# Optimization experiments

Hardware: AMD Instinct MI355X
Metric: run time of the kernel (lower is better)

## Reference

```python
import jax, jax.numpy as jnp
import numpy as np

B, T, I, H = 4096, 512, 3, 64


def setup_inputs() -> dict:
    key = jax.random.key(0)
    ks = jax.random.split(key, 8)
    s = 1.0 / np.sqrt(H)  # PyTorch LSTM init scale
    x = jax.random.normal(ks[0], (B, T, I), dtype=jnp.float32)
    W_ih = jax.random.uniform(ks[1], (4 * H, I), minval=-s, maxval=s, dtype=jnp.float32)
    W_hh = jax.random.uniform(ks[2], (4 * H, H), minval=-s, maxval=s, dtype=jnp.float32)
    b_ih = jax.random.uniform(ks[3], (4 * H,), minval=-s, maxval=s, dtype=jnp.float32)
    b_hh = jax.random.uniform(ks[4], (4 * H,), minval=-s, maxval=s, dtype=jnp.float32)
    W_dec = jax.random.uniform(ks[5], (I, H), minval=-s, maxval=s, dtype=jnp.float32)
    b_dec = jax.random.uniform(ks[6], (I,), minval=-s, maxval=s, dtype=jnp.float32)
    return {"x": x, "W_ih": W_ih, "W_hh": W_hh, "b_ih": b_ih, "b_hh": b_hh,
            "W_dec": W_dec, "b_dec": b_dec}


def _lstm(x, W_ih, W_hh, b_ih, b_hh):
    # Precompute input contribution for all timesteps: [B, T, 4H]
    x_gates = jnp.einsum('bti,gi->btg', x, W_ih) + b_ih + b_hh
    h0 = jnp.zeros((x.shape[0], H), dtype=x.dtype)
    c0 = jnp.zeros((x.shape[0], H), dtype=x.dtype)

    def step(carry, xg_t):
        h, c = carry
        gates = xg_t + h @ W_hh.T  # [B, 4H]
        i_g, f_g, g_g, o_g = jnp.split(gates, 4, axis=-1)  # PyTorch order i,f,g,o
        i_g = jax.nn.sigmoid(i_g)
        f_g = jax.nn.sigmoid(f_g)
        g_g = jnp.tanh(g_g)
        o_g = jax.nn.sigmoid(o_g)
        c_new = f_g * c + i_g * g_g
        h_new = o_g * jnp.tanh(c_new)
        return (h_new, c_new), h_new

    _, hs = jax.lax.scan(step, (h0, c0), jnp.swapaxes(x_gates, 0, 1))  # [T, B, H]
    return jnp.swapaxes(hs, 0, 1)  # [B, T, H]


def reference(x, W_ih, W_hh, b_ih, b_hh, W_dec, b_dec):
    lstm_out = _lstm(x, W_ih, W_hh, b_ih, b_hh)
    return jnp.einsum('bth,oh->bto', lstm_out, W_dec) + b_dec  # [B, T, I]
```

## Files before the change

kernel.cpp:

```cpp
#include <hip/hip_runtime.h>


#define TLEN 512
#define TCHUNK 64
#define ROWS 16

typedef float    float4_t __attribute__((ext_vector_type(4)));
typedef _Float16 halfx8   __attribute__((ext_vector_type(8)));

#define INV2048 4.8828125e-4f

__device__ __forceinline__ float fexp2(float x){ return __builtin_amdgcn_exp2f(x); }
__device__ __forceinline__ float frcp (float x){ return __builtin_amdgcn_rcpf(x); }
__device__ __forceinline__ float sigm (float x){ return frcp(1.f + fexp2(-1.44269504f*x)); }
__device__ __forceinline__ float tanh_(float x){ return 1.f - 2.f*frcp(1.f + fexp2(2.88539008f*x)); }

__device__ __forceinline__ unsigned short hbits(_Float16 h){
  union { _Float16 h; unsigned short u; } x; x.h = h; return x.u;
}

__device__ __forceinline__ void split8h(const float* v, halfx8& hi, halfx8& lo){
  #pragma unroll
  for (int j = 0; j < 8; j++){
    _Float16 h = (_Float16)v[j];
    hi[j] = h;
    lo[j] = (_Float16)((v[j] - (float)h) * 2048.0f);
  }
}

#define MFMA(a,b,c) __builtin_amdgcn_mfma_f32_16x16x32_f16((a),(b),(c),0,0,0)

#define HHI 0
#define HS_SZ 2304
#define XOF 0
#define XPK 3136
#define OOF 7232
#define LF_SZ 10368

__global__ __launch_bounds__(256, 1)
void LSTMAnomalyDetector_kernel(
    const float* __restrict__ x,     const float* __restrict__ W_ih,
    const float* __restrict__ W_hh,  const float* __restrict__ b_ih,
    const float* __restrict__ b_hh,  const float* __restrict__ W_dec,
    const float* __restrict__ b_dec, float* __restrict__ out)
{
  __shared__ __align__(16) unsigned short HS[HS_SZ];
  __shared__ __align__(16) float          LF[LF_SZ];

  const int tid  = threadIdx.x;
  const int w    = tid >> 6;
  const int lane = tid & 63;
  const int q    = lane >> 4;
  const int lid  = lane & 15;
  const int b0   = blockIdx.x * ROWS;
  const int cw   = w*16 + lid;

  halfx8 Bh[4][2], Bl[4][2];
  halfx8 Dh[2];
  float  wi[4][3], bsum[4];

  #pragma unroll
  for (int tl = 0; tl < 4; tl++){
    const int g = tl*64 + cw;
    #pragma unroll
    for (int kt = 0; kt < 2; kt++){
      const float* p = W_hh + g*64 + kt*32 + q*8;
      float v[8];
      #pragma unroll
      for (int j = 0; j < 8; j++) v[j] = p[j];
      split8h(v, Bh[tl][kt], Bl[tl][kt]);
    }
    wi[tl][0] = W_ih[g*3+0];
    wi[tl][1] = W_ih[g*3+1];
    wi[tl][2] = W_ih[g*3+2];
    bsum[tl]  = b_ih[g] + b_hh[g];
  }
  #pragma unroll
  for (int kt = 0; kt < 2; kt++){
    #pragma unroll
    for (int j = 0; j < 8; j++) Dh[kt][j] = (_Float16)0.f;
    if (lid < 3){
      const float* p = W_dec + lid*64 + kt*32 + q*8;
      #pragma unroll
      for (int j = 0; j < 8; j++) Dh[kt][j] = (_Float16)p[j];
    }
  }
  const float bdec = (lid < 3) ? b_dec[lid] : 0.f;

  halfx8 ah0 = {}, ah1 = {};
  float creg[4] = {0.f, 0.f, 0.f, 0.f};
  float4_t xp4[4];

  auto loadx = [&](int d){
    #pragma unroll
    for (int r = 0; r < 4; r++){
      float4_t xv = *(const float4_t*)&LF[XPK + d*64 + (q*4+r)*4];
      #pragma unroll
      for (int tl = 0; tl < 4; tl++)
        xp4[tl][r] = fmaf(wi[tl][2], xv[2],
                      fmaf(wi[tl][1], xv[1],
                        fmaf(wi[tl][0], xv[0], bsum[tl])));
    }
  };

  auto step = [&](int t, int dt, bool last){
    const int hb = (t & 1) * 1152;

    float4_t c1 = xp4[3];
    c1 = MFMA(ah0, Bh[3][0], c1);
    c1 = MFMA(ah1, Bh[3][1], c1);
    float4_t c2 = {0.f,0.f,0.f,0.f};
    c2 = MFMA(ah0, Bl[3][0], c2);
    c2 = MFMA(ah1, Bl[3][1], c2);
    float4_t og;
    #pragma unroll
    for (int r = 0; r < 4; r++) og[r] = sigm(fmaf(c2[r], INV2048, c1[r]));

    c1 = xp4[1];
    c1 = MFMA(ah0, Bh[1][0], c1);
    c1 = MFMA(ah1, Bh[1][1], c1);
    c2 = (float4_t){0.f,0.f,0.f,0.f};
    c2 = MFMA(ah0, Bl[1][0], c2);
    c2 = MFMA(ah1, Bl[1][1], c2);
    float4_t cp;
    #pragma unroll
    for (int r = 0; r < 4; r++){
      const float fg = sigm(fmaf(c2[r], INV2048, c1[r]));
      cp[r] = fg * creg[r];
    }

    c1 = xp4[0];
    c1 = MFMA(ah0, Bh[0][0], c1);
    c1 = MFMA(ah1, Bh[0][1], c1);
    c2 = (float4_t){0.f,0.f,0.f,0.f};
    c2 = MFMA(ah0, Bl[0][0], c2);
    c2 = MFMA(ah1, Bl[0][1], c2);
    float4_t ig;
    #pragma unroll
    for (int r = 0; r < 4; r++) ig[r] = sigm(fmaf(c2[r], INV2048, c1[r]));

    c1 = xp4[2];
    c1 = MFMA(ah0, Bh[2][0], c1);
    c1 = MFMA(ah1, Bh[2][1], c1);
    c2 = (float4_t){0.f,0.f,0.f,0.f};
    c2 = MFMA(ah0, Bl[2][0], c2);
    c2 = MFMA(ah1, Bl[2][1], c2);
    #pragma unroll
    for (int r = 0; r < 4; r++){
      const float gg = tanh_(fmaf(c2[r], INV2048, c1[r]));
      creg[r] = fmaf(ig[r], gg, cp[r]);
      const float h = og[r] * tanh_(creg[r]);
      const _Float16 h16 = (_Float16)h;
      HS[HHI + hb + (q*4+r)*72 + cw] = hbits(h16);
    }

    if (!last) loadx(dt+1);

    __syncthreads();

    {
      const unsigned short* ph = &HS[HHI + hb + lid*72 + q*8];
      ah0 = *(const halfx8*)&ph[0];
      ah1 = *(const halfx8*)&ph[32];
    }

    if (w == 0){
      float4_t d1 = {0.f,0.f,0.f,0.f};
      d1 = MFMA(ah0, Dh[0], d1);
      d1 = MFMA(ah1, Dh[1], d1);
      if (lid < 3){
        #pragma unroll
        for (int r = 0; r < 4; r++)
          LF[OOF + (q*4+r)*196 + dt*3 + lid] = d1[r] + bdec;
      }
    }
  };

  #pragma unroll
  for (int s = 0; s < 3; s++){
    const int f = tid + 256*s;
    const int row = f/48; const int off = (f%48)*4;
    float4_t v = *(const float4_t*)(x + (size_t)(b0+row)*1536 + off);
    *(float4_t*)&LF[XOF + row*196 + off] = v;
  }
  __syncthreads();
  #pragma unroll
  for (int s = 0; s < 4; s++){
    const int p = tid + 256*s;
    const float* xr = &LF[XOF + (p & 15)*196 + (p >> 4)*3];
    float4_t v = {xr[0], xr[1], xr[2], 0.f};
    *(float4_t*)&LF[XPK + p*4] = v;
  }
  __syncthreads();
  loadx(0);

  for (int ck = 0; ck < TLEN/TCHUNK; ++ck){
    const int tb = ck * TCHUNK;

    for (int dt = 0; dt < TCHUNK-1; ++dt)
      step(tb + dt, dt, false);

    step(tb + TCHUNK-1, TCHUNK-1, true);

    __syncthreads();
    #pragma unroll
    for (int s = 0; s < 3; s++){
      const int f = tid + 256*s;
      const int row = f/48; const int off = (f%48)*4;
      float4_t v = *(const float4_t*)&LF[OOF + row*196 + off];
      *(float4_t*)(out + (size_t)(b0+row)*1536 + tb*3 + off) = v;
    }
    if (ck + 1 < TLEN/TCHUNK){
      const int tn = tb + TCHUNK;
      #pragma unroll
      for (int s = 0; s < 3; s++){
        const int f = tid + 256*s;
        const int row = f/48; const int off = (f%48)*4;
        float4_t v = *(const float4_t*)(x + (size_t)(b0+row)*1536 + tn*3 + off);
        *(float4_t*)&LF[XOF + row*196 + off] = v;
      }
      __syncthreads();
      #pragma unroll
      for (int s = 0; s < 4; s++){
        const int p = tid + 256*s;
        const float* xr = &LF[XOF + (p & 15)*196 + (p >> 4)*3];
        float4_t v = {xr[0], xr[1], xr[2], 0.f};
        *(float4_t*)&LF[XPK + p*4] = v;
      }
    }
    __syncthreads();
    if (ck + 1 < TLEN/TCHUNK) loadx(0);
  }
}

extern "C" void kernel_launch(void* const* d_in, const int* in_sizes, int n_in,
                              void* d_out, int out_size, void* d_ws, size_t ws_size,
                              hipStream_t stream)
{
  const float* x     = (const float*)d_in[0];
  const float* W_ih  = (const float*)d_in[1];
  const float* W_hh  = (const float*)d_in[2];
  const float* b_ih  = (const float*)d_in[3];
  const float* b_hh  = (const float*)d_in[4];
  const float* W_dec = (const float*)d_in[5];
  const float* b_dec = (const float*)d_in[6];
  float* out = (float*)d_out;

  const int B = in_sizes[0] / (TLEN * 3);
  const int blocks = B / ROWS;
  hipLaunchKernelGGL(LSTMAnomalyDetector_kernel, dim3(blocks), dim3(256), 0, stream,
                     x, W_ih, W_hh, b_ih, b_hh, W_dec, b_dec, out);
}
```

Measured before the change: 448.0 us.

## Add dedicated decoder warp and double-buffer output to overlap with recurrence

Adds a fifth wavefront that computes the decoder projection for the previous timestep from the shared h buffer, taking that MFMA and store off wave 0's critical path. The output staging area is double-buffered, so a finished chunk is written to global memory lazily at the start of the next chunk instead of at a barrier. In exchange, block size grows to 320 threads and LDS use increases. The extra wave also joins every per-step barrier.

Result: faster. 426.0 us (-4.9%).

```diff
diff --git a/kernel.cpp b/kernel.cpp
--- a/kernel.cpp
+++ b/kernel.cpp
@@ -34,10 +34,11 @@
 #define HS_SZ 2304
 #define XOF 0
 #define XPK 3136
-#define OOF 7232
-#define LF_SZ 10368
-
-__global__ __launch_bounds__(256, 1)
+#define OOF0 7232
+#define OOF1 10368
+#define LF_SZ 13504
+
+__global__ __launch_bounds__(320, 1)
 void LSTMAnomalyDetector_kernel(
     const float* __restrict__ x,     const float* __restrict__ W_ih,
     const float* __restrict__ W_hh,  const float* __restrict__ b_ih,
@@ -53,36 +54,39 @@
   const int q    = lane >> 4;
   const int lid  = lane & 15;
   const int b0   = blockIdx.x * ROWS;
-  const int cw   = w*16 + lid;
+  const int cw   = (w & 3)*16 + lid;
 
   halfx8 Bh[4][2], Bl[4][2];
   halfx8 Dh[2];
   float  wi[4][3], bsum[4];
 
-  #pragma unroll
-  for (int tl = 0; tl < 4; tl++){
-    const int g = tl*64 + cw;
+  if (w < 4){
+    #pragma unroll
+    for (int tl = 0; tl < 4; tl++){
+      const int g = tl*64 + cw;
+      #pragma unroll
+      for (int kt = 0; kt < 2; kt++){
+        const float* p = W_hh + g*64 + kt*32 + q*8;
+        float v[8];
+        #pragma unroll
+        for (int j = 0; j < 8; j++) v[j] = p[j];
+        split8h(v, Bh[tl][kt], Bl[tl][kt]);
+      }
+      wi[tl][0] = W_ih[g*3+0];
+      wi[tl][1] = W_ih[g*3+1];
+      wi[tl][2] = W_ih[g*3+2];
+      bsum[tl]  = b_ih[g] + b_hh[g];
+    }
+  } else {
     #pragma unroll
     for (int kt = 0; kt < 2; kt++){
-      const float* p = W_hh + g*64 + kt*32 + q*8;
-      float v[8];
-      #pragma unroll
-      for (int j = 0; j < 8; j++) v[j] = p[j];
-      split8h(v, Bh[tl][kt], Bl[tl][kt]);
-    }
-    wi[tl][0] = W_ih[g*3+0];
-    wi[tl][1] = W_ih[g*3+1];
-    wi[tl][2] = W_ih[g*3+2];
-    bsum[tl]  = b_ih[g] + b_hh[g];
-  }
-  #pragma unroll
-  for (int kt = 0; kt < 2; kt++){
-    #pragma unroll
-    for (int j = 0; j < 8; j++) Dh[kt][j] = (_Float16)0.f;
-    if (lid < 3){
-      const float* p = W_dec + lid*64 + kt*32 + q*8;
-      #pragma unroll
-      for (int j = 0; j < 8; j++) Dh[kt][j] = (_Float16)p[j];
+      #pragma unroll
+      for (int j = 0; j < 8; j++) Dh[kt][j] = (_Float16)0.f;
+      if (lid < 3){
+        const float* p = W_dec + lid*64 + kt*32 + q*8;
+        #pragma unroll
+        for (int j = 0; j < 8; j++) Dh[kt][j] = (_Float16)p[j];
+      }
     }
   }
   const float bdec = (lid < 3) ? b_dec[lid] : 0.f;
@@ -103,133 +107,177 @@
     }
   };
 
-  auto step = [&](int t, int dt, bool last){
+  if (w < 4){
+    #pragma unroll
+    for (int s = 0; s < 3; s++){
+      const int f = tid + 256*s;
+      const int row = f/48; const int off = (f%48)*4;
+      float4_t v = *(const float4_t*)(x + (size_t)(b0+row)*1536 + off);
+      *(float4_t*)&LF[XOF + row*196 + off] = v;
+    }
+  }
+  __syncthreads();
+  if (w < 4){
+    #pragma unroll
+    for (int s = 0; s < 4; s++){
+      const int p = tid + 256*s;
+      const float* xr = &LF[XOF + (p & 15)*196 + (p >> 4)*3];
+      float4_t v = {xr[0], xr[1], xr[2], 0.f};
+      *(float4_t*)&LF[XPK + p*4] = v;
+    }
+  }
+  __syncthreads();
+  if (w < 4) loadx(0);
+
+  for (int t = 0; t < TLEN; ++t){
+    const int dt = t & (TCHUNK-1);
     const int hb = (t & 1) * 1152;
 
-    float4_t c1 = xp4[3];
-    c1 = MFMA(ah0, Bh[3][0], c1);
-    c1 = MFMA(ah1, Bh[3][1], c1);
-    float4_t c2 = {0.f,0.f,0.f,0.f};
-    c2 = MFMA(ah0, Bl[3][0], c2);
-    c2 = MFMA(ah1, Bl[3][1], c2);
-    float4_t og;
-    #pragma unroll
-    for (int r = 0; r < 4; r++) og[r] = sigm(fmaf(c2[r], INV2048, c1[r]));
-
-    c1 = xp4[1];
-    c1 = MFMA(ah0, Bh[1][0], c1);
-    c1 = MFMA(ah1, Bh[1][1], c1);
-    c2 = (float4_t){0.f,0.f,0.f,0.f};
-    c2 = MFMA(ah0, Bl[1][0], c2);
-    c2 = MFMA(ah1, Bl[1][1], c2);
-    float4_t cp;
-    #pragma unroll
-    for (int r = 0; r < 4; r++){
-      const float fg = sigm(fmaf(c2[r], INV2048, c1[r]));
-      cp[r] = fg * creg[r];
-    }
-
-    c1 = xp4[0];
-    c1 = MFMA(ah0, Bh[0][0], c1);
-    c1 = MFMA(ah1, Bh[0][1], c1);
-    c2 = (float4_t){0.f,0.f,0.f,0.f};
-    c2 = MFMA(ah0, Bl[0][0], c2);
-    c2 = MFMA(ah1, Bl[0][1], c2);
-    float4_t ig;
-    #pragma unroll
-    for (int r = 0; r < 4; r++) ig[r] = sigm(fmaf(c2[r], INV2048, c1[r]));
-
-    c1 = xp4[2];
-    c1 = MFMA(ah0, Bh[2][0], c1);
-    c1 = MFMA(ah1, Bh[2][1], c1);
-    c2 = (float4_t){0.f,0.f,0.f,0.f};
-    c2 = MFMA(ah0, Bl[2][0], c2);
-    c2 = MFMA(ah1, Bl[2][1], c2);
-    #pragma unroll
-    for (int r = 0; r < 4; r++){
-      const float gg = tanh_(fmaf(c2[r], INV2048, c1[r]));
-      creg[r] = fmaf(ig[r], gg, cp[r]);
-      const float h = og[r] * tanh_(creg[r]);
-      const _Float16 h16 = (_Float16)h;
-      HS[HHI + hb + (q*4+r)*72 + cw] = hbits(h16);
-    }
-
-    if (!last) loadx(dt+1);
+    if (w < 4){
+      float4_t c1 = xp4[3];
+      c1 = MFMA(ah0, Bh[3][0], c1);
+      c1 = MFMA(ah1, Bh[3][1], c1);
+      float4_t c2 = {0.f,0.f,0.f,0.f};
+      c2 = MFMA(ah0, Bl[3][0], c2);
+      c2 = MFMA(ah1, Bl[3][1], c2);
+      float4_t og;
+      #pragma unroll
+      for (int r = 0; r < 4; r++) og[r] = sigm(fmaf(c2[r], INV2048, c1[r]));
+
+      c1 = xp4[1];
+      c1 = MFMA(ah0, Bh[1][0], c1);
+      c1 = MFMA(ah1, Bh[1][1], c1);
+      c2 = (float4_t){0.f,0.f,0.f,0.f};
+      c2 = MFMA(ah0, Bl[1][0], c2);
+      c2 = MFMA(ah1, Bl[1][1], c2);
+      float4_t cp;
+      #pragma unroll
+      for (int r = 0; r < 4; r++){
+        const float fg = sigm(fmaf(c2[r], INV2048, c1[r]));
+        cp[r] = fg * creg[r];
+      }
+
+      c1 = xp4[0];
+      c1 = MFMA(ah0, Bh[0][0], c1);
+      c1 = MFMA(ah1, Bh[0][1], c1);
+      c2 = (float4_t){0.f,0.f,0.f,0.f};
+      c2 = MFMA(ah0, Bl[0][0], c2);
+      c2 = MFMA(ah1, Bl[0][1], c2);
+      float4_t ig;
+      #pragma unroll
+      for (int r = 0; r < 4; r++) ig[r] = sigm(fmaf(c2[r], INV2048, c1[r]));
+
+      c1 = xp4[2];
+      c1 = MFMA(ah0, Bh[2][0], c1);
+      c1 = MFMA(ah1, Bh[2][1], c1);
+      c2 = (float4_t){0.f,0.f,0.f,0.f};
+      c2 = MFMA(ah0, Bl[2][0], c2);
+      c2 = MFMA(ah1, Bl[2][1], c2);
+      #pragma unroll
+      for (int r = 0; r < 4; r++){
+        const float gg = tanh_(fmaf(c2[r], INV2048, c1[r]));
+        creg[r] = fmaf(ig[r], gg, cp[r]);
+        const float h = og[r] * tanh_(creg[r]);
+        const _Float16 h16 = (_Float16)h;
+        HS[HHI + hb + (q*4+r)*72 + cw] = hbits(h16);
+      }
+
+      if (dt != TCHUNK-1) loadx(dt+1);
+    } else {
+      if (t > 0){
+        const int hbp = (1 - (t & 1)) * 1152;
+        const unsigned short* ph = &HS[HHI + hbp + lid*72 + q*8];
+        halfx8 dh0 = *(const halfx8*)&ph[0];
+        halfx8 dh1 = *(const halfx8*)&ph[32];
+        float4_t d1 = {0.f,0.f,0.f,0.f};
+        d1 = MFMA(dh0, Dh[0], d1);
+        d1 = MFMA(dh1, Dh[1], d1);
+        if (lid < 3){
+          const int tp  = t - 1;
+          const int oof = OOF0 + ((tp >> 6) & 1) * 3136;
+          const int dto = tp & (TCHUNK-1);
+          #pragma unroll
+          for (int r = 0; r < 4; r++)
+            LF[oof + (q*4+r)*196 + dto*3 + lid] = d1[r] + bdec;
+        }
+      }
+    }
 
     __syncthreads();
 
-    {
+    if (w < 4){
       const unsigned short* ph = &HS[HHI + hb + lid*72 + q*8];
       ah0 = *(const halfx8*)&ph[0];
       ah1 = *(const halfx8*)&ph[32];
-    }
-
-    if (w == 0){
-      float4_t d1 = {0.f,0.f,0.f,0.f};
-      d1 = MFMA(ah0, Dh[0], d1);
-      d1 = MFMA(ah1, Dh[1], d1);
-      if (lid < 3){
+
+      if (dt == 1 && t > TCHUNK){
+        const int ckf = (t >> 6) - 1;
+        const int oof = OOF0 + (ckf & 1) * 3136;
+        const int t0  = ckf * TCHUNK;
         #pragma unroll
-        for (int r = 0; r < 4; r++)
-          LF[OOF + (q*4+r)*196 + dt*3 + lid] = d1[r] + bdec;
-      }
-    }
-  };
-
-  #pragma unroll
-  for (int s = 0; s < 3; s++){
-    const int f = tid + 256*s;
-    const int row = f/48; const int off = (f%48)*4;
-    float4_t v = *(const float4_t*)(x + (size_t)(b0+row)*1536 + off);
-    *(float4_t*)&LF[XOF + row*196 + off] = v;
+        for (int s = 0; s < 3; s++){
+          const int f = tid + 256*s;
+          const int row = f/48; const int off = (f%48)*4;
+          float4_t v = *(const float4_t*)&LF[oof + row*196 + off];
+          *(float4_t*)(out + (size_t)(b0+row)*1536 + t0*3 + off) = v;
+        }
+      }
+    }
+
+    if (dt == TCHUNK-1){
+      if (t + 1 < TLEN){
+        if (w < 4){
+          #pragma unroll
+          for (int s = 0; s < 3; s++){
+            const int f = tid + 256*s;
+            const int row = f/48; const int off = (f%48)*4;
+            float4_t v = *(const float4_t*)(x + (size_t)(b0+row)*1536 + (t+1)*3 + off);
+            *(float4_t*)&LF[XOF + row*196 + off] = v;
+          }
+        }
+        __syncthreads();
+        if (w < 4){
+          #pragma unroll
+          for (int s = 0; s < 4; s++){
+            const int p = tid + 256*s;
+            const float* xr = &LF[XOF + (p & 15)*196 + (p >> 4)*3];
+            float4_t v = {xr[0], xr[1], xr[2], 0.f};
+            *(float4_t*)&LF[XPK + p*4] = v;
+          }
+        }
+      }
+      __syncthreads();
+      if (w < 4 && t + 1 < TLEN) loadx(0);
+    }
+  }
+
+  if (w == 4){
+    const int hbp = ((TLEN-1) & 1) * 1152;
+    const unsigned short* ph = &HS[HHI + hbp + lid*72 + q*8];
+    halfx8 dh0 = *(const halfx8*)&ph[0];
+    halfx8 dh1 = *(const halfx8*)&ph[32];
+    float4_t d1 = {0.f,0.f,0.f,0.f};
+    d1 = MFMA(dh0, Dh[0], d1);
+    d1 = MFMA(dh1, Dh[1], d1);
+    if (lid < 3){
+      const int oof = OOF0 + (((TLEN-1) >> 6) & 1) * 3136;
+      #pragma unroll
+      for (int r = 0; r < 4; r++)
+        LF[oof + (q*4+r)*196 + 63*3 + lid] = d1[r] + bdec;
+    }
   }
   __syncthreads();
-  #pragma unroll
-  for (int s = 0; s < 4; s++){
-    const int p = tid + 256*s;
-    const float* xr = &LF[XOF + (p & 15)*196 + (p >> 4)*3];
-    float4_t v = {xr[0], xr[1], xr[2], 0.f};
-    *(float4_t*)&LF[XPK + p*4] = v;
-  }
-  __syncthreads();
-  loadx(0);
-
-  for (int ck = 0; ck < TLEN/TCHUNK; ++ck){
-    const int tb = ck * TCHUNK;
-
-    for (int dt = 0; dt < TCHUNK-1; ++dt)
-      step(tb + dt, dt, false);
-
-    step(tb + TCHUNK-1, TCHUNK-1, true);
-
-    __syncthreads();
+  if (w < 4){
+    const int ckf = (TLEN >> 6) - 1;
+    const int oof = OOF0 + (ckf & 1) * 3136;
+    const int t0  = ckf * TCHUNK;
     #pragma unroll
     for (int s = 0; s < 3; s++){
       const int f = tid + 256*s;
       const int row = f/48; const int off = (f%48)*4;
-      float4_t v = *(const float4_t*)&LF[OOF + row*196 + off];
-      *(float4_t*)(out + (size_t)(b0+row)*1536 + tb*3 + off) = v;
-    }
-    if (ck + 1 < TLEN/TCHUNK){
-      const int tn = tb + TCHUNK;
-      #pragma unroll
-      for (int s = 0; s < 3; s++){
-        const int f = tid + 256*s;
-        const int row = f/48; const int off = (f%48)*4;
-        float4_t v = *(const float4_t*)(x + (size_t)(b0+row)*1536 + tn*3 + off);
-        *(float4_t*)&LF[XOF + row*196 + off] = v;
-      }
-      __syncthreads();
-      #pragma unroll
-      for (int s = 0; s < 4; s++){
-        const int p = tid + 256*s;
-        const float* xr = &LF[XOF + (p & 15)*196 + (p >> 4)*3];
-        float4_t v = {xr[0], xr[1], xr[2], 0.f};
-        *(float4_t*)&LF[XPK + p*4] = v;
-      }
-    }
-    __syncthreads();
-    if (ck + 1 < TLEN/TCHUNK) loadx(0);
+      float4_t v = *(const float4_t*)&LF[oof + row*196 + off];
+      *(float4_t*)(out + (size_t)(b0+row)*1536 + t0*3 + off) = v;
+    }
   }
 }
 
@@ -248,6 +296,6 @@
 
   const int B = in_sizes[0] / (TLEN * 3);
   const int blocks = B / ROWS;
-  hipLaunchKernelGGL(LSTMAnomalyDetector_kernel, dim3(blocks), dim3(256), 0, stream,
+  hipLaunchKernelGGL(LSTMAnomalyDetector_kernel, dim3(blocks), dim3(320), 0, stream,
                      x, W_ih, W_hh, b_ih, b_hh, W_dec, b_dec, out);
 }
```
